# Kernel tuning notes

Measured on AMD Instinct MI355X. Metric: run time of the kernel, lower is better.

## Reference

```python
import jax, jax.numpy as jnp
import numpy as np

QSIGN = jnp.array([1.0, -1.0, -1.0, -1.0], dtype=jnp.float32)
IDENT = jnp.array([1.0, 0.0, 0.0, 0.0], dtype=jnp.float32)


def quat_multiply(a, b):
    aw, ax, ay, az = a[..., 0], a[..., 1], a[..., 2], a[..., 3]
    bw, bx, by, bz = b[..., 0], b[..., 1], b[..., 2], b[..., 3]
    return jnp.stack([
        aw * bw - ax * bx - ay * by - az * bz,
        aw * bx + ax * bw + ay * bz - az * by,
        aw * by - ax * bz + ay * bw + az * bx,
        aw * bz + ax * by - ay * bx + az * bw], axis=-1)


def quat_to_rot(q):
    w, x, y, z = q[..., 0], q[..., 1], q[..., 2], q[..., 3]
    r = jnp.stack([
        w * w + x * x - y * y - z * z, 2 * (x * y - w * z), 2 * (x * z + w * y),
        2 * (x * y + w * z), w * w - x * x + y * y - z * z, 2 * (y * z - w * x),
        2 * (x * z - w * y), 2 * (y * z + w * x), w * w - x * x - y * y + z * z], axis=-1)
    return r.reshape(q.shape[:-1] + (3, 3))


def quat_rotate(q, v):
    return jnp.einsum('...ij,...j->...i', quat_to_rot(q), v)


def mlp(z, W1, b1, W2, b2):
    return jax.nn.relu(z @ W1 + b1) @ W2 + b2


def setup_inputs() -> dict:
    key = jax.random.key(0)
    ks = jax.random.split(key, 24)
    B, N, H, E, M, O, T = 2, 512, 64, 32, 64, 64, 64
    x = jax.random.normal(ks[0], (B, N, 3), dtype=jnp.float32)
    q = jax.random.normal(ks[1], (B, N, 4), dtype=jnp.float32)
    q = q / jnp.linalg.norm(q, axis=-1, keepdims=True)  # unit quats
    h = jax.random.normal(ks[2], (B, N, H), dtype=jnp.float32)
    e = jax.random.normal(ks[3], (B, N, N, E), dtype=jnp.float32)
    node_mask = jnp.ones((B, N), dtype=bool)

    def lin(k, fi, fo):
        return jax.random.normal(k, (fi, fo), dtype=jnp.float32) / np.sqrt(fi)

    msg_in = 2 * H + E + 9  # 169
    inp = dict(x=x, quats=q, h=h, e=e, node_mask=node_mask,
               Wm1=lin(ks[4], msg_in, T), bm1=jnp.zeros((T,)),
               Wm2=lin(ks[5], T, M), bm2=jnp.zeros((M,)),
               Wf1=lin(ks[6], H + M, T), bf1=jnp.zeros((T,)),
               Wf2=lin(ks[7], T, O), bf2=jnp.zeros((O,)),
               Wt1=lin(ks[8], M, T), bt1=jnp.zeros((T,)),
               Wt2=lin(ks[9], T, 3), bt2=jnp.zeros((3,)),
               Wq1=lin(ks[10], M, T), bq1=jnp.zeros((T,)),
               Wq2=lin(ks[11], T, 4), bq2=jnp.zeros((4,)))
    return inp


def reference(x, quats, h, e, node_mask,
              Wm1, bm1, Wm2, bm2, Wf1, bf1, Wf2, bf2,
              Wt1, bt1, Wt2, bt2, Wq1, bq1, Wq2, bq2):
    B, N, H = h.shape
    eye = jnp.eye(N, dtype=bool)[None]
    msg_mask = node_mask[:, :, None] & node_mask[:, None, :] & ~eye  # [B,N,N]
    n_nodes = node_mask.sum(axis=-1).astype(x.dtype)  # [B]

    # inverse frame of node j: rot = conj(q_j)/|q_j|^2, applied as R_j^-1 (x_i - t_j)
    q_inv = (quats * QSIGN) / jnp.sum(quats * quats, axis=-1, keepdims=True)

    diff = x[:, :, None, :] - x[:, None, :, :]            # [B,N,N,3], x_i - x_j
    d2 = jnp.sum(diff * diff, axis=-1)                    # [B,N,N]
    qdot = jnp.abs(jnp.einsum('bik,bjk->bij', quats, quats))
    local_x = quat_rotate(q_inv[:, None, :, :], diff)     # R_j^-1 (x_i - x_j)
    local_q = quat_multiply(q_inv[:, None, :, :], quats[:, :, None, :])  # q_j^-1 * q_i

    hi = jnp.broadcast_to(h[:, :, None, :], (B, N, N, H))
    hj = jnp.broadcast_to(h[:, None, :, :], (B, N, N, H))
    feat = jnp.concatenate([hi, hj, e, local_x, local_q,
                            d2[..., None], qdot[..., None]], axis=-1)

    m = mlp(feat, Wm1, bm1, Wm2, bm2) * msg_mask[..., None]  # [B,N,N,M]
    msum = m.sum(axis=-2)                                    # [B,N,M]

    o = mlp(jnp.concatenate([h, msum], axis=-1), Wf1, bf1, Wf2, bf2)

    dx = mlp(m, Wt1, bt1, Wt2, bt2) * msg_mask[..., None]    # [B,N,N,3]

    dq = mlp(msum, Wq1, bq1, Wq2, bq2)                       # [B,N,4]
    dq = jnp.where(node_mask[..., None], dq, IDENT)
    dq = dq / jnp.maximum(jnp.linalg.norm(dq, axis=-1, keepdims=True), 1e-12)

    upd_q = quat_multiply(quats, dq)
    upd_q = jnp.where(node_mask[..., None], upd_q, IDENT)
    upd_q = upd_q / jnp.linalg.norm(upd_q, axis=-1, keepdims=True)  # normalize_quats=True

    # rotate dx[i,j] by updated frame of node j, aggregate over j
    rot_dx = quat_rotate(upd_q[:, None, :, :], dx).sum(axis=-2)     # [B,N,3]
    upd_x = x + rot_dx / (n_nodes[:, None, None] - 1.0)
    return upd_q, upd_x, o
```

## Files before the change

kernel.cpp:

```cpp
#include <hip/hip_runtime.h>
#include <math.h>
#include <stdint.h>

#define B_ 2
#define N_ 512

#define WS_NGEO  0
#define WS_APRE  8192
#define WS_BPREF 73728
#define WS_MPART 139264
#define WS_DXBUF 401408

typedef short short8v __attribute__((ext_vector_type(8)));
typedef float f32x4 __attribute__((ext_vector_type(4)));

union FragU { int4 i; short8v s; };
union PackU { uint32_t w[4]; short8v s; };

static __device__ inline uint32_t pk2(float lo, float hi) {
    uint32_t r;
    asm volatile("v_cvt_pk_bf16_f32 %0, %1, %2" : "=v"(r) : "v"(lo), "v"(hi));
    return r;
}
static __device__ inline short f2bs(float f) {
    uint32_t u = __float_as_uint(f);
    u = (u + 0x7FFFu + ((u >> 16) & 1u)) >> 16;
    return (short)u;
}

__global__ __launch_bounds__(256) void k_node_pre(
    const float* __restrict__ x,
    const float* __restrict__ quats,
    const float* __restrict__ h,
    const float* __restrict__ Wm1,
    const float* __restrict__ bm1,
    float* __restrict__ ngeo,
    float* __restrict__ Apre,
    float* __restrict__ BpreF)
{
    __shared__ float sW[128 * 64];
    __shared__ float sh[4][64];

    const int tid = threadIdx.x;
    for (int idx = tid; idx < 128 * 64 / 4; idx += 256)
        ((float4*)sW)[idx] = ((const float4*)Wm1)[idx];

    const int wv = tid >> 6;
    const int c = tid & 63;
    const int node = blockIdx.x * 4 + wv;

    sh[wv][c] = h[node * 64 + c];
    __syncthreads();

    float a = bm1[c];
    float bv = 0.f;
#pragma unroll 8
    for (int k = 0; k < 64; ++k) {
        const float hk = sh[wv][k];
        a  = fmaf(hk, sW[k * 64 + c], a);
        bv = fmaf(hk, sW[(64 + k) * 64 + c], bv);
    }
    Apre[node * 64 + c] = a;
    const int aa = c >> 4, gg = (c >> 2) & 3, bb = c & 3;
    BpreF[(node >> 4) * 1024 + ((node & 15) + 16 * gg) * 16 + 4 * aa + bb] = bv;

    if (c == 0) {
        ngeo[node * 8 + 0] = x[node * 3 + 0];
        ngeo[node * 8 + 1] = x[node * 3 + 1];
        ngeo[node * 8 + 2] = x[node * 3 + 2];
        ngeo[node * 8 + 3] = 0.f;
        ngeo[node * 8 + 4] = quats[node * 4 + 0];
        ngeo[node * 8 + 5] = quats[node * 4 + 1];
        ngeo[node * 8 + 6] = quats[node * 4 + 2];
        ngeo[node * 8 + 7] = quats[node * 4 + 3];
    }
}

__global__ __launch_bounds__(256, 3) void k_edge(
    const float* __restrict__ e,
    const float* __restrict__ ngeo,
    const float* __restrict__ Apre,
    const float* __restrict__ BpreF,
    const float* __restrict__ Wm1, const float* __restrict__ Wm2,
    const float* __restrict__ bm2,
    const float* __restrict__ Wt1, const float* __restrict__ bt1,
    const float* __restrict__ Wt2, const float* __restrict__ bt2,
    float* __restrict__ mpart, float* __restrict__ dxbuf)
{
    __shared__ short W1s[64 * 72];
    __shared__ short W2s[64 * 72];
    __shared__ short W3s[64 * 72];
    __shared__ short W4s[16 * 72];

    const int tid = threadIdx.x;

    for (int idx = tid; idx < 64 * 72; idx += 256) {
        const int ch = idx / 72, p = idx % 72;
        float v1 = 0.f, v2 = 0.f, v3 = 0.f;
        if (p < 64) {
            if (p < 32) v1 = Wm1[(128 + p) * 64 + ch];
            else if (p < 41) v1 = Wm1[(160 + p - 32) * 64 + ch];
            const int s = p >> 5, ee = p & 7, gg = (p >> 3) & 3;
            const int k1 = 32 * s + 16 * (ee >> 2) + 4 * gg + (ee & 3);
            v2 = Wm2[k1 * 64 + ch];
            v3 = Wt1[k1 * 64 + ch];
        }
        W1s[idx] = f2bs(v1); W2s[idx] = f2bs(v2); W3s[idx] = f2bs(v3);
    }
    for (int idx = tid; idx < 16 * 72; idx += 256) {
        const int d = idx / 72, p = idx % 72;
        float v = 0.f;
        if (p < 64 && d < 3) {
            const int s = p >> 5, ee = p & 7, gg = (p >> 3) & 3;
            const int k1 = 32 * s + 16 * (ee >> 2) + 4 * gg + (ee & 3);
            v = Wt2[k1 * 3 + d];
        }
        W4s[idx] = f2bs(v);
    }
    __syncthreads();

    const int w = tid >> 6;
    const int l = tid & 63;
    const int g = l >> 4;
    const int c = l & 15;

    const int ig = blockIdx.x >> 2;
    const int quarter = blockIdx.x & 3;
    const int ni = ig * 4 + w;
    const int b = ni >> 9;
    const int i = ni & 511;
    const int j0w = quarter * 128;

    const float4 gi0 = ((const float4*)ngeo)[ni * 2 + 0];
    const float4 gi1 = ((const float4*)ngeo)[ni * 2 + 1];
    const float xi0 = gi0.x, xi1 = gi0.y, xi2 = gi0.z;
    const float qi0 = gi1.x, qi1 = gi1.y, qi2 = gi1.z, qi3 = gi1.w;

    float apre[16], bm2r[16], bt1r[16], bt2r[4];
#pragma unroll
    for (int q = 0; q < 16; ++q) {
        const int row = 16 * (q >> 2) + 4 * g + (q & 3);
        apre[q] = Apre[ni * 64 + row];
        bm2r[q] = bm2[row];
        bt1r[q] = bt1[row];
    }
#pragma unroll
    for (int q = 0; q < 4; ++q) {
        const int d = 4 * g + q;
        bt2r[q] = (d < 3) ? bt2[d] : 0.f;
    }

    float msum[16];
#pragma unroll
    for (int q = 0; q < 16; ++q) msum[q] = 0.f;

#pragma unroll 2
    for (int t = 0; t < 8; ++t) {
        const int j0m = j0w + t * 16;
        const int nj = b * N_ + j0m + c;

        const float* ep = e + ((size_t)(b * N_ + i) * N_ + j0m + c) * 32 + g * 8;
        const float4 e0 = *(const float4*)ep;
        const float4 e1 = *(const float4*)(ep + 4);
        const float4 n0 = ((const float4*)ngeo)[nj * 2 + 0];
        const float4 n1 = ((const float4*)ngeo)[nj * 2 + 1];
        const float* bp = BpreF + (size_t)(nj >> 4) * 1024 + l * 16;
        const float4 bi0 = ((const float4*)bp)[0];
        const float4 bi1 = ((const float4*)bp)[1];
        const float4 bi2 = ((const float4*)bp)[2];
        const float4 bi3 = ((const float4*)bp)[3];

        const float xj0 = n0.x, xj1 = n0.y, xj2 = n0.z;
        const float qj0 = n1.x, qj1 = n1.y, qj2 = n1.z, qj3 = n1.w;
        const float dsum = qj0 * qj0 + qj1 * qj1 + qj2 * qj2 + qj3 * qj3;
        const float inv = __builtin_amdgcn_rcpf(dsum);
        const float qw = qj0 * inv, qx = -qj1 * inv;
        const float qy = -qj2 * inv, qz = -qj3 * inv;
        const float d0 = xi0 - xj0, d1 = xi1 - xj1, d2v = xi2 - xj2;
        const float dd = d0 * d0 + d1 * d1 + d2v * d2v;
        const float qd = fabsf(qi0 * qj0 + qi1 * qj1 + qi2 * qj2 + qi3 * qj3);
        const float ww = qw * qw, xx = qx * qx, yy = qy * qy, zz = qz * qz;
        const float xy = qx * qy, xz = qx * qz, yz = qy * qz;
        const float wx = qw * qx, wy = qw * qy, wz = qw * qz;
        const float lx0 = (ww + xx - yy - zz) * d0 + 2.f * (xy - wz) * d1 + 2.f * (xz + wy) * d2v;
        const float lx1 = 2.f * (xy + wz) * d0 + (ww - xx + yy - zz) * d1 + 2.f * (yz - wx) * d2v;
        const float lx2 = 2.f * (xz - wy) * d0 + 2.f * (yz + wx) * d1 + (ww - xx - yy + zz) * d2v;
        const float lq0 = qw * qi0 - qx * qi1 - qy * qi2 - qz * qi3;
        const float lq1 = qw * qi1 + qx * qi0 + qy * qi3 - qz * qi2;
        const float lq2 = qw * qi2 - qx * qi3 + qy * qi0 + qz * qi1;
        const float lq3 = qw * qi3 + qx * qi2 - qy * qi1 + qz * qi0;

        PackU y0, yg;
        y0.w[0] = pk2(e0.x, e0.y); y0.w[1] = pk2(e0.z, e0.w);
        y0.w[2] = pk2(e1.x, e1.y); y0.w[3] = pk2(e1.z, e1.w);
        const uint32_t w0 = pk2(lx0, lx1), w1 = pk2(lx2, lq0);
        const uint32_t w2 = pk2(lq1, lq2), w3 = pk2(lq3, dd);
        const uint32_t wq = pk2(qd, 0.f);
        yg.w[0] = (g == 0) ? w0 : ((g == 1) ? wq : 0u);
        yg.w[1] = (g == 0) ? w1 : 0u;
        yg.w[2] = (g == 0) ? w2 : 0u;
        yg.w[3] = (g == 0) ? w3 : 0u;

        f32x4 acc1[4];
        acc1[0][0] = apre[0] + bi0.x;  acc1[0][1] = apre[1] + bi0.y;
        acc1[0][2] = apre[2] + bi0.z;  acc1[0][3] = apre[3] + bi0.w;
        acc1[1][0] = apre[4] + bi1.x;  acc1[1][1] = apre[5] + bi1.y;
        acc1[1][2] = apre[6] + bi1.z;  acc1[1][3] = apre[7] + bi1.w;
        acc1[2][0] = apre[8] + bi2.x;  acc1[2][1] = apre[9] + bi2.y;
        acc1[2][2] = apre[10] + bi2.z; acc1[2][3] = apre[11] + bi2.w;
        acc1[3][0] = apre[12] + bi3.x; acc1[3][1] = apre[13] + bi3.y;
        acc1[3][2] = apre[14] + bi3.z; acc1[3][3] = apre[15] + bi3.w;
#pragma unroll
        for (int nt = 0; nt < 4; ++nt) {
            FragU xw0, xw1;
            xw0.i = *(const int4*)&W1s[(16 * nt + c) * 72 + g * 8];
            xw1.i = *(const int4*)&W1s[(16 * nt + c) * 72 + 32 + g * 8];
            acc1[nt] = __builtin_amdgcn_mfma_f32_16x16x32_bf16(xw0.s, y0.s, acc1[nt], 0, 0, 0);
            acc1[nt] = __builtin_amdgcn_mfma_f32_16x16x32_bf16(xw1.s, yg.s, acc1[nt], 0, 0, 0);
        }

        PackU by1[2];
#pragma unroll
        for (int s = 0; s < 2; ++s) {
            const f32x4 a0 = acc1[2 * s], a1 = acc1[2 * s + 1];
            by1[s].w[0] = pk2(fmaxf(a0[0], 0.f), fmaxf(a0[1], 0.f));
            by1[s].w[1] = pk2(fmaxf(a0[2], 0.f), fmaxf(a0[3], 0.f));
            by1[s].w[2] = pk2(fmaxf(a1[0], 0.f), fmaxf(a1[1], 0.f));
            by1[s].w[3] = pk2(fmaxf(a1[2], 0.f), fmaxf(a1[3], 0.f));
        }

        f32x4 acc2[4];
#pragma unroll
        for (int nt = 0; nt < 4; ++nt) {
            acc2[nt][0] = bm2r[nt * 4 + 0]; acc2[nt][1] = bm2r[nt * 4 + 1];
            acc2[nt][2] = bm2r[nt * 4 + 2]; acc2[nt][3] = bm2r[nt * 4 + 3];
        }
#pragma unroll
        for (int nt = 0; nt < 4; ++nt)
#pragma unroll
            for (int s = 0; s < 2; ++s) {
                FragU xw;
                xw.i = *(const int4*)&W2s[(16 * nt + c) * 72 + s * 32 + g * 8];
                acc2[nt] = __builtin_amdgcn_mfma_f32_16x16x32_bf16(
                    xw.s, by1[s].s, acc2[nt], 0, 0, 0);
            }

        const float maskf = (j0m + c == i) ? 0.f : 1.f;
#pragma unroll
        for (int nt = 0; nt < 4; ++nt) {
            acc2[nt][0] *= maskf; acc2[nt][1] *= maskf;
            acc2[nt][2] *= maskf; acc2[nt][3] *= maskf;
            msum[nt * 4 + 0] += acc2[nt][0];
            msum[nt * 4 + 1] += acc2[nt][1];
            msum[nt * 4 + 2] += acc2[nt][2];
            msum[nt * 4 + 3] += acc2[nt][3];
        }

        PackU by2[2];
#pragma unroll
        for (int s = 0; s < 2; ++s) {
            const f32x4 a0 = acc2[2 * s], a1 = acc2[2 * s + 1];
            by2[s].w[0] = pk2(a0[0], a0[1]);
            by2[s].w[1] = pk2(a0[2], a0[3]);
            by2[s].w[2] = pk2(a1[0], a1[1]);
            by2[s].w[3] = pk2(a1[2], a1[3]);
        }

        f32x4 acc3[4];
#pragma unroll
        for (int nt = 0; nt < 4; ++nt) {
            acc3[nt][0] = bt1r[nt * 4 + 0]; acc3[nt][1] = bt1r[nt * 4 + 1];
            acc3[nt][2] = bt1r[nt * 4 + 2]; acc3[nt][3] = bt1r[nt * 4 + 3];
        }
#pragma unroll
        for (int nt = 0; nt < 4; ++nt)
#pragma unroll
            for (int s = 0; s < 2; ++s) {
                FragU xw;
                xw.i = *(const int4*)&W3s[(16 * nt + c) * 72 + s * 32 + g * 8];
                acc3[nt] = __builtin_amdgcn_mfma_f32_16x16x32_bf16(
                    xw.s, by2[s].s, acc3[nt], 0, 0, 0);
            }

        PackU by3[2];
#pragma unroll
        for (int s = 0; s < 2; ++s) {
            const f32x4 a0 = acc3[2 * s], a1 = acc3[2 * s + 1];
            by3[s].w[0] = pk2(fmaxf(a0[0], 0.f), fmaxf(a0[1], 0.f));
            by3[s].w[1] = pk2(fmaxf(a0[2], 0.f), fmaxf(a0[3], 0.f));
            by3[s].w[2] = pk2(fmaxf(a1[0], 0.f), fmaxf(a1[1], 0.f));
            by3[s].w[3] = pk2(fmaxf(a1[2], 0.f), fmaxf(a1[3], 0.f));
        }

        f32x4 acc4;
        acc4[0] = bt2r[0]; acc4[1] = bt2r[1]; acc4[2] = bt2r[2]; acc4[3] = bt2r[3];
#pragma unroll
        for (int s = 0; s < 2; ++s) {
            FragU xw;
            xw.i = *(const int4*)&W4s[c * 72 + s * 32 + g * 8];
            acc4 = __builtin_amdgcn_mfma_f32_16x16x32_bf16(
                xw.s, by3[s].s, acc4, 0, 0, 0);
        }
        if (g == 0) {
            float4 o4;
            o4.x = acc4[0] * maskf; o4.y = acc4[1] * maskf;
            o4.z = acc4[2] * maskf; o4.w = 0.f;
            ((float4*)dxbuf)[(size_t)ni * N_ + j0m + c] = o4;
        }
    }

#pragma unroll
    for (int q = 0; q < 16; ++q) {
        float v = msum[q];
        v += __shfl_xor(v, 1); v += __shfl_xor(v, 2);
        v += __shfl_xor(v, 4); v += __shfl_xor(v, 8);
        msum[q] = v;
    }
    if (c == 0) {
#pragma unroll
        for (int nt = 0; nt < 4; ++nt) {
            float4 mo;
            mo.x = msum[nt * 4 + 0]; mo.y = msum[nt * 4 + 1];
            mo.z = msum[nt * 4 + 2]; mo.w = msum[nt * 4 + 3];
            *(float4*)&mpart[((size_t)(quarter * (B_ * N_) + ni)) * 64 + 16 * nt + 4 * g] = mo;
        }
    }
}

__global__ __launch_bounds__(256) void k_node_post(
    const float* __restrict__ quats,
    const float* __restrict__ h,
    const float* __restrict__ mpart,
    const float* __restrict__ Wf1, const float* __restrict__ bf1,
    const float* __restrict__ Wf2, const float* __restrict__ bf2,
    const float* __restrict__ Wq1, const float* __restrict__ bq1,
    const float* __restrict__ Wq2, const float* __restrict__ bq2,
    float* __restrict__ out_q, float* __restrict__ out_o)
{
    __shared__ float sWf1[128 * 64];
    __shared__ float sWf2[64 * 64];
    __shared__ float sWq1[64 * 64];
    __shared__ float sWq2[64 * 4];
    __shared__ float sh[4][64], sm[4][64], stf[4][64], stq[4][64];

    const int tid = threadIdx.x;
    for (int idx = tid; idx < 128 * 64 / 4; idx += 256)
        ((float4*)sWf1)[idx] = ((const float4*)Wf1)[idx];
    for (int idx = tid; idx < 64 * 64 / 4; idx += 256) {
        ((float4*)sWf2)[idx] = ((const float4*)Wf2)[idx];
        ((float4*)sWq1)[idx] = ((const float4*)Wq1)[idx];
    }
    if (tid < 64) {
        sWq2[tid * 4 + 0] = Wq2[tid * 4 + 0];
        sWq2[tid * 4 + 1] = Wq2[tid * 4 + 1];
        sWq2[tid * 4 + 2] = Wq2[tid * 4 + 2];
        sWq2[tid * 4 + 3] = Wq2[tid * 4 + 3];
    }

    const int wv = tid >> 6;
    const int c = tid & 63;
    const int node = blockIdx.x * 4 + wv;

    const float ms = mpart[(size_t)node * 64 + c] +
                     mpart[((size_t)(B_ * N_) + node) * 64 + c] +
                     mpart[((size_t)(2 * B_ * N_) + node) * 64 + c] +
                     mpart[((size_t)(3 * B_ * N_) + node) * 64 + c];
    sm[wv][c] = ms;
    sh[wv][c] = h[node * 64 + c];
    __syncthreads();

    float accf = bf1[c];
    float accq = bq1[c];
#pragma unroll 8
    for (int k = 0; k < 64; ++k) {
        const float hk = sh[wv][k];
        const float mk = sm[wv][k];
        accf = fmaf(hk, sWf1[k * 64 + c], accf);
        accf = fmaf(mk, sWf1[(64 + k) * 64 + c], accf);
        accq = fmaf(mk, sWq1[k * 64 + c], accq);
    }
    stf[wv][c] = fmaxf(accf, 0.f);
    stq[wv][c] = fmaxf(accq, 0.f);
    __syncthreads();

    float o = bf2[c];
#pragma unroll 8
    for (int k = 0; k < 64; ++k) o = fmaf(stf[wv][k], sWf2[k * 64 + c], o);
    out_o[(size_t)node * 64 + c] = o;

    {
        const int d = c & 3, kb = c >> 2;
        float p = 0.f;
#pragma unroll
        for (int m = 0; m < 4; ++m) {
            const int kk = kb + 16 * m;
            p = fmaf(stq[wv][kk], sWq2[kk * 4 + d], p);
        }
        p += __shfl_xor(p, 4);  p += __shfl_xor(p, 8);
        p += __shfl_xor(p, 16); p += __shfl_xor(p, 32);
        const float p0 = __shfl(p, 0), p1 = __shfl(p, 1);
        const float p2 = __shfl(p, 2), p3 = __shfl(p, 3);
        if (c == 0) {
            float dq0 = p0 + bq2[0], dq1 = p1 + bq2[1];
            float dq2 = p2 + bq2[2], dq3 = p3 + bq2[3];
            const float nrm = sqrtf(dq0 * dq0 + dq1 * dq1 + dq2 * dq2 + dq3 * dq3);
            const float inv = 1.f / fmaxf(nrm, 1e-12f);
            const float b0 = dq0 * inv, b1 = dq1 * inv, b2 = dq2 * inv, b3 = dq3 * inv;
            const float aw = quats[node * 4 + 0], ax = quats[node * 4 + 1];
            const float ay = quats[node * 4 + 2], az = quats[node * 4 + 3];
            float u0 = aw * b0 - ax * b1 - ay * b2 - az * b3;
            float u1 = aw * b1 + ax * b0 + ay * b3 - az * b2;
            float u2 = aw * b2 - ax * b3 + ay * b0 + az * b1;
            float u3 = aw * b3 + ax * b2 - ay * b1 + az * b0;
            const float n2 = sqrtf(u0 * u0 + u1 * u1 + u2 * u2 + u3 * u3);
            u0 /= n2; u1 /= n2; u2 /= n2; u3 /= n2;
            out_q[node * 4 + 0] = u0; out_q[node * 4 + 1] = u1;
            out_q[node * 4 + 2] = u2; out_q[node * 4 + 3] = u3;
        }
    }
}

__global__ void k_aggregate(const float* __restrict__ x,
                            const float* __restrict__ out_q,
                            const float* __restrict__ dxbuf,
                            float* __restrict__ out_x)
{
    const int node = blockIdx.x;
    const int b = node >> 9;
    const int tid = threadIdx.x;

    float s0 = 0.f, s1 = 0.f, s2 = 0.f;
    for (int j = tid; j < N_; j += 256) {
        const float4 d4 = ((const float4*)dxbuf)[(size_t)node * N_ + j];
        const float4 q4 = ((const float4*)out_q)[b * N_ + j];
        const float w = q4.x, X = q4.y, Y = q4.z, Z = q4.w;
        const float ww = w * w, xx = X * X, yy = Y * Y, zz = Z * Z;
        const float xy = X * Y, xz = X * Z, yz = Y * Z;
        const float wx = w * X, wy = w * Y, wz = w * Z;
        s0 += (ww + xx - yy - zz) * d4.x + 2.f * (xy - wz) * d4.y + 2.f * (xz + wy) * d4.z;
        s1 += 2.f * (xy + wz) * d4.x + (ww - xx + yy - zz) * d4.y + 2.f * (yz - wx) * d4.z;
        s2 += 2.f * (xz - wy) * d4.x + 2.f * (yz + wx) * d4.y + (ww - xx - yy + zz) * d4.z;
    }
#pragma unroll
    for (int off = 1; off <= 32; off <<= 1) {
        s0 += __shfl_xor(s0, off);
        s1 += __shfl_xor(s1, off);
        s2 += __shfl_xor(s2, off);
    }
    __shared__ float red[4][3];
    const int wave = tid >> 6, lane = tid & 63;
    if (lane == 0) { red[wave][0] = s0; red[wave][1] = s1; red[wave][2] = s2; }
    __syncthreads();
    if (tid == 0) {
        const float t0 = red[0][0] + red[1][0] + red[2][0] + red[3][0];
        const float t1 = red[0][1] + red[1][1] + red[2][1] + red[3][1];
        const float t2 = red[0][2] + red[1][2] + red[2][2] + red[3][2];
        const float inv = 1.f / (float)(N_ - 1);
        out_x[node * 3 + 0] = x[node * 3 + 0] + t0 * inv;
        out_x[node * 3 + 1] = x[node * 3 + 1] + t1 * inv;
        out_x[node * 3 + 2] = x[node * 3 + 2] + t2 * inv;
    }
}

extern "C" void kernel_launch(void* const* d_in, const int* in_sizes, int n_in,
                              void* d_out, int out_size, void* d_ws, size_t ws_size,
                              hipStream_t stream) {
    const float* x     = (const float*)d_in[0];
    const float* quats = (const float*)d_in[1];
    const float* h     = (const float*)d_in[2];
    const float* e     = (const float*)d_in[3];
    const float* Wm1 = (const float*)d_in[5];
    const float* bm1 = (const float*)d_in[6];
    const float* Wm2 = (const float*)d_in[7];
    const float* bm2 = (const float*)d_in[8];
    const float* Wf1 = (const float*)d_in[9];
    const float* bf1 = (const float*)d_in[10];
    const float* Wf2 = (const float*)d_in[11];
    const float* bf2 = (const float*)d_in[12];
    const float* Wt1 = (const float*)d_in[13];
    const float* bt1 = (const float*)d_in[14];
    const float* Wt2 = (const float*)d_in[15];
    const float* bt2 = (const float*)d_in[16];
    const float* Wq1 = (const float*)d_in[17];
    const float* bq1 = (const float*)d_in[18];
    const float* Wq2 = (const float*)d_in[19];
    const float* bq2 = (const float*)d_in[20];

    float* out = (float*)d_out;
    float* out_q = out;
    float* out_x = out + 4096;
    float* out_o = out + 7168;

    float* ws    = (float*)d_ws;
    float* ngeo  = ws + WS_NGEO;
    float* Apre  = ws + WS_APRE;
    float* BpreF = ws + WS_BPREF;
    float* mpart = ws + WS_MPART;
    float* dxbuf = ws + WS_DXBUF;

    k_node_pre<<<dim3(B_ * N_ / 4), dim3(256), 0, stream>>>(
        x, quats, h, Wm1, bm1, ngeo, Apre, BpreF);

    k_edge<<<dim3(1024), dim3(256), 0, stream>>>(
        e, ngeo, Apre, BpreF, Wm1, Wm2, bm2, Wt1, bt1, Wt2, bt2,
        mpart, dxbuf);

    k_node_post<<<dim3(B_ * N_ / 4), dim3(256), 0, stream>>>(
        quats, h, mpart, Wf1, bf1, Wf2, bf2, Wq1, bq1, Wq2, bq2,
        out_q, out_o);

    k_aggregate<<<dim3(B_ * N_), dim3(256), 0, stream>>>(
        x, out_q, dxbuf, out_x);
}
```

Measured before the change: 211.5 us.

## Pre-convert edge MLP weights to bf16 once and use 512-thread edge blocks

Adds a small prep kernel that converts and permutes the edge MLP weights into a bf16 workspace buffer once per call. Each edge block then loads them with vectorized int4 copies instead of every block redoing scattered fp32 loads and conversions. The edge kernel now uses 512 threads per block covering two column quarters, halving the number of blocks. It also combines two partial message sums through LDS, so mpart shrinks from four partials to two. The cost is an extra kernel launch and extra block-level barriers.

```diff
diff --git a/kernel.cpp b/kernel.cpp
--- a/kernel.cpp
+++ b/kernel.cpp
@@ -5,11 +5,12 @@
 #define B_ 2
 #define N_ 512
 
-#define WS_NGEO  0
-#define WS_APRE  8192
-#define WS_BPREF 73728
-#define WS_MPART 139264
-#define WS_DXBUF 401408
+#define WS_WBF   0
+#define WS_NGEO  7680
+#define WS_APRE  15872
+#define WS_BPREF 81408
+#define WS_MPART 146944
+#define WS_DXBUF 278016
 
 typedef short short8v __attribute__((ext_vector_type(8)));
 typedef float f32x4 __attribute__((ext_vector_type(4)));
@@ -26,6 +27,38 @@
     uint32_t u = __float_as_uint(f);
     u = (u + 0x7FFFu + ((u >> 16) & 1u)) >> 16;
     return (short)u;
+}
+
+__global__ void k_prep(const float* __restrict__ Wm1, const float* __restrict__ Wm2,
+                       const float* __restrict__ Wt1, const float* __restrict__ Wt2,
+                       short* __restrict__ wbf)
+{
+    const int id = blockIdx.x * 256 + threadIdx.x;
+    if (id < 4608) {
+        const int ch = id / 72, p = id % 72;
+        float v1 = 0.f, v2 = 0.f, v3 = 0.f;
+        if (p < 64) {
+            if (p < 32) v1 = Wm1[(128 + p) * 64 + ch];
+            else if (p < 41) v1 = Wm1[(160 + p - 32) * 64 + ch];
+            const int s = p >> 5, ee = p & 7, gg = (p >> 3) & 3;
+            const int k1 = 32 * s + 16 * (ee >> 2) + 4 * gg + (ee & 3);
+            v2 = Wm2[k1 * 64 + ch];
+            v3 = Wt1[k1 * 64 + ch];
+        }
+        wbf[id] = f2bs(v1);
+        wbf[4608 + id] = f2bs(v2);
+        wbf[9216 + id] = f2bs(v3);
+    } else if (id < 5760) {
+        const int idx = id - 4608;
+        const int d = idx / 72, p = idx % 72;
+        float v = 0.f;
+        if (p < 64 && d < 3) {
+            const int s = p >> 5, ee = p & 7, gg = (p >> 3) & 3;
+            const int k1 = 32 * s + 16 * (ee >> 2) + 4 * gg + (ee & 3);
+            v = Wt2[k1 * 3 + d];
+        }
+        wbf[13824 + idx] = f2bs(v);
+    }
 }
 
 __global__ __launch_bounds__(256) void k_node_pre(
@@ -76,59 +109,42 @@
     }
 }
 
-__global__ __launch_bounds__(256, 3) void k_edge(
+__global__ __launch_bounds__(512, 4) void k_edge(
     const float* __restrict__ e,
     const float* __restrict__ ngeo,
     const float* __restrict__ Apre,
     const float* __restrict__ BpreF,
-    const float* __restrict__ Wm1, const float* __restrict__ Wm2,
+    const short* __restrict__ wbf,
     const float* __restrict__ bm2,
-    const float* __restrict__ Wt1, const float* __restrict__ bt1,
-    const float* __restrict__ Wt2, const float* __restrict__ bt2,
+    const float* __restrict__ bt1,
+    const float* __restrict__ bt2,
     float* __restrict__ mpart, float* __restrict__ dxbuf)
 {
-    __shared__ short W1s[64 * 72];
-    __shared__ short W2s[64 * 72];
-    __shared__ short W3s[64 * 72];
-    __shared__ short W4s[16 * 72];
+    __shared__ __align__(16) short Ws[14976];
+    __shared__ float msLDS[4][64];
 
     const int tid = threadIdx.x;
 
-    for (int idx = tid; idx < 64 * 72; idx += 256) {
-        const int ch = idx / 72, p = idx % 72;
-        float v1 = 0.f, v2 = 0.f, v3 = 0.f;
-        if (p < 64) {
-            if (p < 32) v1 = Wm1[(128 + p) * 64 + ch];
-            else if (p < 41) v1 = Wm1[(160 + p - 32) * 64 + ch];
-            const int s = p >> 5, ee = p & 7, gg = (p >> 3) & 3;
-            const int k1 = 32 * s + 16 * (ee >> 2) + 4 * gg + (ee & 3);
-            v2 = Wm2[k1 * 64 + ch];
-            v3 = Wt1[k1 * 64 + ch];
-        }
-        W1s[idx] = f2bs(v1); W2s[idx] = f2bs(v2); W3s[idx] = f2bs(v3);
-    }
-    for (int idx = tid; idx < 16 * 72; idx += 256) {
-        const int d = idx / 72, p = idx % 72;
-        float v = 0.f;
-        if (p < 64 && d < 3) {
-            const int s = p >> 5, ee = p & 7, gg = (p >> 3) & 3;
-            const int k1 = 32 * s + 16 * (ee >> 2) + 4 * gg + (ee & 3);
-            v = Wt2[k1 * 3 + d];
-        }
-        W4s[idx] = f2bs(v);
-    }
-    __syncthreads();
+    for (int idx = tid; idx < 1872; idx += 512)
+        ((int4*)Ws)[idx] = ((const int4*)wbf)[idx];
+    __syncthreads();
+
+    const short* W1s = Ws;
+    const short* W2s = Ws + 4608;
+    const short* W3s = Ws + 9216;
+    const short* W4s = Ws + 13824;
 
     const int w = tid >> 6;
     const int l = tid & 63;
     const int g = l >> 4;
     const int c = l & 15;
 
-    const int ig = blockIdx.x >> 2;
-    const int quarter = blockIdx.x & 3;
-    const int ni = ig * 4 + w;
+    const int ig = blockIdx.x >> 1;
+    const int half = blockIdx.x & 1;
+    const int ni = ig * 4 + (w >> 1);
     const int b = ni >> 9;
     const int i = ni & 511;
+    const int quarter = half * 2 + (w & 1);
     const int j0w = quarter * 128;
 
     const float4 gi0 = ((const float4*)ngeo)[ni * 2 + 0];
@@ -316,13 +332,22 @@
         v += __shfl_xor(v, 4); v += __shfl_xor(v, 8);
         msum[q] = v;
     }
-    if (c == 0) {
+    __syncthreads();
+    if ((w & 1) && c == 0) {
+#pragma unroll
+        for (int q = 0; q < 16; ++q)
+            msLDS[w >> 1][16 * (q >> 2) + 4 * g + (q & 3)] = msum[q];
+    }
+    __syncthreads();
+    if (!(w & 1) && c == 0) {
 #pragma unroll
         for (int nt = 0; nt < 4; ++nt) {
             float4 mo;
-            mo.x = msum[nt * 4 + 0]; mo.y = msum[nt * 4 + 1];
-            mo.z = msum[nt * 4 + 2]; mo.w = msum[nt * 4 + 3];
-            *(float4*)&mpart[((size_t)(quarter * (B_ * N_) + ni)) * 64 + 16 * nt + 4 * g] = mo;
+            mo.x = msum[nt * 4 + 0] + msLDS[w >> 1][16 * nt + 4 * g + 0];
+            mo.y = msum[nt * 4 + 1] + msLDS[w >> 1][16 * nt + 4 * g + 1];
+            mo.z = msum[nt * 4 + 2] + msLDS[w >> 1][16 * nt + 4 * g + 2];
+            mo.w = msum[nt * 4 + 3] + msLDS[w >> 1][16 * nt + 4 * g + 3];
+            *(float4*)&mpart[((size_t)(half * (B_ * N_) + ni)) * 64 + 16 * nt + 4 * g] = mo;
         }
     }
 }
@@ -362,9 +387,7 @@
     const int node = blockIdx.x * 4 + wv;
 
     const float ms = mpart[(size_t)node * 64 + c] +
-                     mpart[((size_t)(B_ * N_) + node) * 64 + c] +
-                     mpart[((size_t)(2 * B_ * N_) + node) * 64 + c] +
-                     mpart[((size_t)(3 * B_ * N_) + node) * 64 + c];
+                     mpart[((size_t)(B_ * N_) + node) * 64 + c];
     sm[wv][c] = ms;
     sh[wv][c] = h[node * 64 + c];
     __syncthreads();
@@ -492,18 +515,20 @@
     float* out_o = out + 7168;
 
     float* ws    = (float*)d_ws;
+    short* wbf   = (short*)(ws + WS_WBF);
     float* ngeo  = ws + WS_NGEO;
     float* Apre  = ws + WS_APRE;
     float* BpreF = ws + WS_BPREF;
     float* mpart = ws + WS_MPART;
     float* dxbuf = ws + WS_DXBUF;
 
+    k_prep<<<dim3(23), dim3(256), 0, stream>>>(Wm1, Wm2, Wt1, Wt2, wbf);
+
     k_node_pre<<<dim3(B_ * N_ / 4), dim3(256), 0, stream>>>(
         x, quats, h, Wm1, bm1, ngeo, Apre, BpreF);
 
-    k_edge<<<dim3(1024), dim3(256), 0, stream>>>(
-        e, ngeo, Apre, BpreF, Wm1, Wm2, bm2, Wt1, bt1, Wt2, bt2,
-        mpart, dxbuf);
+    k_edge<<<dim3(512), dim3(512), 0, stream>>>(
+        e, ngeo, Apre, BpreF, wbf, bm2, bt1, bt2, mpart, dxbuf);
 
     k_node_post<<<dim3(B_ * N_ / 4), dim3(256), 0, stream>>>(
         quats, h, mpart, Wf1, bf1, Wf2, bf2, Wq1, bq1, Wq2, bq2,
```

New measurement: 256.1 us. 21.1% more time.
